# Optimization experiments

Hardware: AMD Instinct MI355X
Metric: run time of the kernel (lower is better)

The kernel has to match this reference:

```python
import jax, jax.numpy as jnp
import numpy as np

DIM = 1024
INTER = 512
E = 32            # n_routed_experts
TOPK = 4          # n_activated_experts
GROUPS = 8        # n_expert_groups
TOPK_GROUPS = 4
SHARED_INTER = 2 * INTER  # n_shared_experts * moe_inter_dim
ROUTE_SCALE = 1.0
B, S = 8, 4096


def setup_inputs() -> dict:
    key = jax.random.key(0)
    ks = jax.random.split(key, 16)
    def xav(k, shape):
        fan_in, fan_out = shape[-2], shape[-1]
        lim = np.sqrt(6.0 / (fan_in + fan_out))
        return jax.random.uniform(k, shape, jnp.float32, -lim, lim)
    return {
        "x": jax.random.normal(ks[0], (B, S, DIM), jnp.float32),
        "gw": xav(ks[1], (DIM, E)),
        "gb": jnp.zeros((E,), jnp.float32),
        "w1": xav(ks[2], (E, DIM, INTER)),
        "b1": jnp.zeros((E, INTER), jnp.float32),
        "w3": xav(ks[3], (E, DIM, INTER)),
        "b3": jnp.zeros((E, INTER), jnp.float32),
        "w2": xav(ks[4], (E, INTER, DIM)),
        "b2": jnp.zeros((E, DIM), jnp.float32),
        "sw1": xav(ks[5], (DIM, SHARED_INTER)),
        "sb1": jnp.zeros((SHARED_INTER,), jnp.float32),
        "sw3": xav(ks[6], (DIM, SHARED_INTER)),
        "sb3": jnp.zeros((SHARED_INTER,), jnp.float32),
        "sw2": xav(ks[7], (SHARED_INTER, DIM)),
        "sb2": jnp.zeros((DIM,), jnp.float32),
    }


def _gate(xf, gw, gb):
    # scores: softmax over routed experts in fp32 (score_func='softmax')
    T = xf.shape[0]
    scores = jax.nn.softmax((xf @ gw + gb).astype(jnp.float32), axis=-1)  # [T, E]
    original_scores = scores
    # group-masked routing (n_expert_groups > 1)
    scores_g = scores.reshape(T, GROUPS, E // GROUPS)                     # [T, G, E/G]
    group_scores = jnp.sum(jax.lax.top_k(scores_g, 2)[0], axis=-1)        # [T, G]
    gidx = jax.lax.top_k(group_scores, TOPK_GROUPS)[1]                    # [T, topk_groups]
    keep = jnp.zeros((T, GROUPS), bool).at[jnp.arange(T)[:, None], gidx].set(True)
    masked = jnp.where(keep[:, :, None], scores_g, -jnp.inf).reshape(T, E)
    indices = jax.lax.top_k(masked, TOPK)[1]                              # [T, topk]
    weights = jnp.take_along_axis(original_scores, indices, axis=1) * ROUTE_SCALE
    return weights.astype(xf.dtype), indices


def reference(x, gw, gb, w1, b1, w3, b3, w2, b2, sw1, sb1, sw3, sb3, sw2, sb2):
    shape = x.shape
    xf = x.reshape(-1, DIM)                                               # [T, dim]
    T = xf.shape[0]
    weights, indices = _gate(xf, gw, gb)
    # dense combine weights [T, E]: w_e(t) = routing weight if expert e chosen for t else 0
    cw = jnp.zeros((T, E), xf.dtype).at[jnp.arange(T)[:, None], indices].add(weights)
    # scan over experts: y += w_e * SwiGLU_e(x). Zero weight -> zero contribution,
    # identical math to the masked dispatch/scatter-add in the torch code.
    def body(y, p):
        w1e, b1e, w3e, b3e, w2e, b2e, we = p
        h = jax.nn.silu(xf @ w1e + b1e) * (xf @ w3e + b3e)                # [T, inter]
        return y + we[:, None] * (h @ w2e + b2e), None
    y0 = jnp.zeros_like(xf)
    y, _ = jax.lax.scan(body, y0, (w1, b1, w3, b3, w2, b2, cw.T))
    # shared experts MLP (SwiGLU)
    z = (jax.nn.silu(xf @ sw1 + sb1) * (xf @ sw3 + sb3)) @ sw2 + sb2
    return (y + z).reshape(shape)
```

## Files before the change

kernel.cpp:

```cpp
#include <hip/hip_runtime.h>
#include <stdint.h>

#define DIM_    1024
#define INTER_  512

typedef short bf16x4 __attribute__((ext_vector_type(4)));
typedef short bf16x8 __attribute__((ext_vector_type(8)));
typedef float f32x4  __attribute__((ext_vector_type(4)));

__device__ __forceinline__ unsigned short f2bf(float f) {
  union { float f; unsigned u; } v; v.f = f;
  return (unsigned short)((v.u + 0x7FFFu + ((v.u >> 16) & 1u)) >> 16);
}
__device__ __forceinline__ unsigned f2bf2(float a, float b) {
  union { float f; unsigned u; } va, vb; va.f = a; vb.f = b;
  unsigned ra = (va.u + 0x7FFFu + ((va.u >> 16) & 1u)) >> 16;
  unsigned rb = (vb.u + 0x7FFFu + ((vb.u >> 16) & 1u)) >> 16;
  return ra | (rb << 16);
}
__device__ __forceinline__ float bfhi(unsigned u) {
  union { unsigned u; float f; } v; v.u = u & 0xffff0000u; return v.f;
}
__device__ __forceinline__ float bflo(unsigned u) {
  union { unsigned u; float f; } v; v.u = u << 16; return v.f;
}
__device__ __forceinline__ int xorB(int j) { return (j & 7) ^ ((j >> 3) & 7); }

__device__ __forceinline__ void gl16(const void* g, void* l) {
  __builtin_amdgcn_global_load_lds(
      (const __attribute__((address_space(1))) unsigned int*)g,
      (__attribute__((address_space(3))) unsigned int*)l, 16, 0, 0);
}

__global__ __launch_bounds__(256) void gate_kernel(
    const float* __restrict__ x, const float* __restrict__ gw,
    const float* __restrict__ gb, int* __restrict__ idx, float* __restrict__ wts) {
  __shared__ double s_sc[4][32];
  __shared__ double s_gs[4][8];
  const int wid = threadIdx.x >> 6, lane = threadIdx.x & 63;
  const int t = blockIdx.x * 4 + wid;
  const int e = lane & 31, half = lane >> 5;
  const float* xr  = x  + (size_t)t * DIM_ + half * 512;
  const float* gwp = gw + (size_t)half * 512 * 32 + e;
  double a0 = 0, a1 = 0, a2 = 0, a3 = 0;
  for (int k = 0; k < 512; k += 4) {
    float4 xv = *(const float4*)(xr + k);
    a0 += (double)xv.x * (double)gwp[(k + 0) * 32];
    a1 += (double)xv.y * (double)gwp[(k + 1) * 32];
    a2 += (double)xv.z * (double)gwp[(k + 2) * 32];
    a3 += (double)xv.w * (double)gwp[(k + 3) * 32];
  }
  double lg = (a0 + a1) + (a2 + a3);
  lg += __shfl_xor(lg, 32);
  lg += (double)gb[e];
  double m = lg;
  #pragma unroll
  for (int d = 1; d < 32; d <<= 1) m = fmax(m, __shfl_xor(m, d));
  double ex = exp(lg - m);
  double ssum = ex;
  #pragma unroll
  for (int d = 1; d < 32; d <<= 1) ssum += __shfl_xor(ssum, d);
  double sc = ex / ssum;
  double p  = __shfl_xor(sc, 1);
  double m1 = fmax(sc, p), n1 = fmin(sc, p);
  double m2 = __shfl_xor(m1, 2), n2 = __shfl_xor(n1, 2);
  double gs = (m1 >= m2) ? (m1 + fmax(n1, m2)) : (m2 + fmax(n2, m1));
  if (lane < 32) {
    s_sc[wid][e] = sc;
    if ((e & 3) == 0) s_gs[wid][e >> 2] = gs;
  }
  __syncthreads();
  if (lane == 0) {
    unsigned kmask = 0;
    for (int it = 0; it < 4; ++it) {
      int bg = 0; double bv = -1.0;
      for (int g = 0; g < 8; ++g)
        if (!((kmask >> g) & 1u) && s_gs[wid][g] > bv) { bv = s_gs[wid][g]; bg = g; }
      kmask |= 1u << bg;
    }
    unsigned umask = 0;
    for (int slot = 0; slot < 4; ++slot) {
      int be = 0; double bv = -1.0;
      for (int ee = 0; ee < 32; ++ee)
        if (((kmask >> (ee >> 2)) & 1u) && !((umask >> ee) & 1u) && s_sc[wid][ee] > bv) {
          bv = s_sc[wid][ee]; be = ee;
        }
      umask |= 1u << be;
      idx[t * 4 + slot] = be;
      wts[t * 4 + slot] = (float)bv;
    }
  }
}

__global__ __launch_bounds__(256) void count_kernel(const int* __restrict__ idx,
                                                    int* __restrict__ meta) {
  __shared__ int h[32];
  int tid = threadIdx.x;
  if (tid < 32) h[tid] = 0;
  __syncthreads();
  atomicAdd(&h[idx[blockIdx.x * 256 + tid]], 1);
  __syncthreads();
  if (tid < 32 && h[tid]) atomicAdd(&meta[tid], h[tid]);
}

__global__ void scan_kernel(int* __restrict__ meta) {
  int lane = threadIdx.x & 63;
  if (lane < 32) {
    int c = meta[lane];
    int pre = c;
    #pragma unroll
    for (int d = 1; d < 32; d <<= 1) { int t = __shfl_up(pre, d); if (lane >= d) pre += t; }
    int excl = pre - c;
    meta[64 + lane] = excl;
    meta[32 + lane] = excl;
    int nt = (c + 127) >> 7;
    int ntp = nt;
    #pragma unroll
    for (int d = 1; d < 32; d <<= 1) { int t = __shfl_up(ntp, d); if (lane >= d) ntp += t; }
    int ntExcl = ntp - nt;
    for (int k = 0; k < nt; ++k) { meta[128 + ntExcl + k] = lane; meta[1184 + ntExcl + k] = k << 7; }
    if (lane == 31) { meta[96] = excl + c; meta[97] = ntExcl + nt; }
  }
}

__global__ __launch_bounds__(256) void scatter_kernel(
    const int* __restrict__ idx, int* __restrict__ meta,
    int* __restrict__ tok, int* __restrict__ inv) {
  int i = blockIdx.x * 256 + threadIdx.x;
  int lane = threadIdx.x & 63;
  int e = idx[i];
  unsigned long long m = ~0ull;
  #pragma unroll
  for (int b = 0; b < 5; ++b) {
    unsigned long long vote = __ballot((e >> b) & 1);
    m &= ((e >> b) & 1) ? vote : ~vote;
  }
  int leader = __ffsll((long long)m) - 1;
  int rank = __popcll(m & ((1ull << lane) - 1));
  int base = 0;
  if (lane == leader) base = atomicAdd(&meta[32 + e], (int)__popcll(m));
  base = __shfl(base, leader);
  int p = base + rank;
  tok[p] = i >> 2;
  inv[i] = p;
}

__global__ __launch_bounds__(256) void cvt_x_kernel(const float* __restrict__ x,
                                                    unsigned short* __restrict__ xb) {
  size_t i = ((size_t)blockIdx.x * 256 + threadIdx.x) * 8;
  float4 f0 = *(const float4*)(x + i);
  float4 f1 = *(const float4*)(x + i + 4);
  uint4 o;
  o.x = f2bf2(f0.x, f0.y); o.y = f2bf2(f0.z, f0.w);
  o.z = f2bf2(f1.x, f1.y); o.w = f2bf2(f1.z, f1.w);
  *(uint4*)(xb + i) = o;
}

__global__ __launch_bounds__(256) void repack_kernel(
    const float* __restrict__ src, unsigned short* __restrict__ dst,
    int K, int N, int tilesPerMat) {
  const int w = blockIdx.x * 4 + (threadIdx.x >> 6);
  const int l = threadIdx.x & 63;
  const int e = w / tilesPerMat, rem = w % tilesPerMat;
  const int kSteps = K >> 5;
  const int nt = rem / kSteps, kq = rem % kSteps;
  const float* s = src + (size_t)e * K * N + (size_t)(kq * 32) * N + nt * 64 + l;
  float v[32];
  #pragma unroll
  for (int kk = 0; kk < 32; ++kk) v[kk] = s[(size_t)kk * N];
  char* d = (char*)dst + (size_t)w * 4096 + l * 64;
  const int xb_ = xorB(l);
  #pragma unroll
  for (int q = 0; q < 8; ++q) {
    uint2 o;
    o.x = f2bf2(v[4 * q + 0], v[4 * q + 1]);
    o.y = f2bf2(v[4 * q + 2], v[4 * q + 3]);
    *(uint2*)(d + ((q ^ xb_) << 3)) = o;
  }
}

__global__ __launch_bounds__(256) void s1_kernel(
    const unsigned short* __restrict__ xb, const unsigned short* __restrict__ b1i,
    const unsigned short* __restrict__ b3i, const float* __restrict__ sb1,
    const float* __restrict__ sb3, unsigned short* __restrict__ Hs) {
  __shared__ char lds[32768];
  const int n0 = blockIdx.x * 64;
  const int m0 = blockIdx.y * 128;
  const int tid = threadIdx.x, lane = tid & 63, wave = tid >> 6;
  const int wm = wave >> 1, wn = wave & 1;

  const int r0 = tid >> 2, s0 = tid & 3;
  const int vrw = (r0 & 3) ^ ((r0 >> 2) & 1);
  const char* a0 = (const char*)xb + (size_t)(m0 + r0) * 2048 + ((s0 ^ vrw) << 4);
  const char* a1 = (const char*)xb + (size_t)(m0 + r0 + 64) * 2048 + ((s0 ^ vrw) << 4);
  const char* b1p = (const char*)b1i + (size_t)(blockIdx.x * 32) * 4096 + tid * 16;
  const char* b3p = (const char*)b3i + (size_t)(blockIdx.x * 32) * 4096 + tid * 16;

  const int g = lane >> 4;
  const int vfr = (lane & 3) ^ ((lane >> 2) & 1);
  const int aro = (wm * 64 + (lane & 15)) * 64 + ((g ^ vfr) << 4);
  int bofs[2];
  #pragma unroll
  for (int ni = 0; ni < 2; ++ni) {
    int j = wn * 32 + ni * 16 + (lane & 15);
    bofs[ni] = j * 64 + (((2 * g) ^ xorB(j)) << 3);
  }

  f32x4 acc1[4][2], acc3[4][2];
  const f32x4 zz = {0.f, 0.f, 0.f, 0.f};
  #pragma unroll
  for (int mi = 0; mi < 4; ++mi)
    #pragma unroll
    for (int ni = 0; ni < 2; ++ni) { acc1[mi][ni] = zz; acc3[mi][ni] = zz; }

  auto stage = [&](int buf, int kq) {
    char* b = lds + buf * 16384;
    gl16(a0 + kq * 64, b + wave * 1024);
    gl16(a1 + kq * 64, b + 4096 + wave * 1024);
    gl16(b1p + (size_t)kq * 4096, b + 8192 + wave * 1024);
    gl16(b3p + (size_t)kq * 4096, b + 12288 + wave * 1024);
  };
  stage(0, 0);
  __syncthreads();
  int cur = 0;
  for (int kq = 0; kq < 32; ++kq) {
    if (kq + 1 < 32) stage(cur ^ 1, kq + 1);
    char* cb = lds + cur * 16384;
    bf16x8 af[4];
    #pragma unroll
    for (int mi = 0; mi < 4; ++mi) af[mi] = *(const bf16x8*)(cb + aro + mi * 1024);
    #pragma unroll
    for (int ni = 0; ni < 2; ++ni) {
      bf16x4 lo = *(const bf16x4*)(cb + 8192 + bofs[ni]);
      bf16x4 hi = *(const bf16x4*)(cb + 8192 + (bofs[ni] ^ 8));
      bf16x8 bv = __builtin_shufflevector(lo, hi, 0, 1, 2, 3, 4, 5, 6, 7);
      #pragma unroll
      for (int mi = 0; mi < 4; ++mi)
        acc1[mi][ni] = __builtin_amdgcn_mfma_f32_16x16x32_bf16(af[mi], bv, acc1[mi][ni], 0, 0, 0);
      bf16x4 lo3 = *(const bf16x4*)(cb + 12288 + bofs[ni]);
      bf16x4 hi3 = *(const bf16x4*)(cb + 12288 + (bofs[ni] ^ 8));
      bf16x8 bv3 = __builtin_shufflevector(lo3, hi3, 0, 1, 2, 3, 4, 5, 6, 7);
      #pragma unroll
      for (int mi = 0; mi < 4; ++mi)
        acc3[mi][ni] = __builtin_amdgcn_mfma_f32_16x16x32_bf16(af[mi], bv3, acc3[mi][ni], 0, 0, 0);
    }
    __syncthreads();
    cur ^= 1;
  }
  #pragma unroll
  for (int ni = 0; ni < 2; ++ni) {
    int col = n0 + wn * 32 + ni * 16 + (lane & 15);
    float bb1 = sb1[col], bb3 = sb3[col];
    #pragma unroll
    for (int mi = 0; mi < 4; ++mi) {
      int rb = wm * 64 + mi * 16 + ((lane >> 4) << 2);
      #pragma unroll
      for (int r = 0; r < 4; ++r) {
        int row = m0 + rb + r;
        float v1 = acc1[mi][ni][r] + bb1;
        float v3 = acc3[mi][ni][r] + bb3;
        float h = (v1 / (1.f + __expf(-v1))) * v3;
        Hs[(size_t)row * 1024 + col] = f2bf(h);
      }
    }
  }
}

__global__ __launch_bounds__(256) void s2_kernel(
    const unsigned short* __restrict__ Hs, const unsigned short* __restrict__ b2i,
    const float* __restrict__ sb2, float* __restrict__ out) {
  __shared__ char lds[32768];
  const int n0 = blockIdx.x * 128;
  const int m0 = blockIdx.y * 128;
  const int tid = threadIdx.x, lane = tid & 63, wave = tid >> 6;
  const int wm = wave >> 1, wn = wave & 1;

  const int r0 = tid >> 2, s0 = tid & 3;
  const int vrw = (r0 & 3) ^ ((r0 >> 2) & 1);
  const char* a0 = (const char*)Hs + (size_t)(m0 + r0) * 2048 + ((s0 ^ vrw) << 4);
  const char* a1 = (const char*)Hs + (size_t)(m0 + r0 + 64) * 2048 + ((s0 ^ vrw) << 4);
  const char* bp0 = (const char*)b2i + (size_t)((blockIdx.x * 2 + 0) * 32) * 4096 + tid * 16;
  const char* bp1 = (const char*)b2i + (size_t)((blockIdx.x * 2 + 1) * 32) * 4096 + tid * 16;

  const int g = lane >> 4;
  const int vfr = (lane & 3) ^ ((lane >> 2) & 1);
  const int aro = (wm * 64 + (lane & 15)) * 64 + ((g ^ vfr) << 4);
  int bofs[4];
  #pragma unroll
  for (int ni = 0; ni < 4; ++ni) {
    int j = wn * 64 + ni * 16 + (lane & 15);
    bofs[ni] = j * 64 + (((2 * g) ^ xorB(j)) << 3);
  }
  f32x4 acc[4][4];
  const f32x4 zz = {0.f, 0.f, 0.f, 0.f};
  #pragma unroll
  for (int mi = 0; mi < 4; ++mi)
    #pragma unroll
    for (int ni = 0; ni < 4; ++ni) acc[mi][ni] = zz;

  auto stage = [&](int buf, int kq) {
    char* b = lds + buf * 16384;
    gl16(a0 + kq * 64, b + wave * 1024);
    gl16(a1 + kq * 64, b + 4096 + wave * 1024);
    gl16(bp0 + (size_t)kq * 4096, b + 8192 + wave * 1024);
    gl16(bp1 + (size_t)kq * 4096, b + 12288 + wave * 1024);
  };
  stage(0, 0);
  __syncthreads();
  int cur = 0;
  for (int kq = 0; kq < 32; ++kq) {
    if (kq + 1 < 32) stage(cur ^ 1, kq + 1);
    char* cb = lds + cur * 16384;
    bf16x8 af[4];
    #pragma unroll
    for (int mi = 0; mi < 4; ++mi) af[mi] = *(const bf16x8*)(cb + aro + mi * 1024);
    #pragma unroll
    for (int ni = 0; ni < 4; ++ni) {
      bf16x4 lo = *(const bf16x4*)(cb + 8192 + bofs[ni]);
      bf16x4 hi = *(const bf16x4*)(cb + 8192 + (bofs[ni] ^ 8));
      bf16x8 bv = __builtin_shufflevector(lo, hi, 0, 1, 2, 3, 4, 5, 6, 7);
      #pragma unroll
      for (int mi = 0; mi < 4; ++mi)
        acc[mi][ni] = __builtin_amdgcn_mfma_f32_16x16x32_bf16(af[mi], bv, acc[mi][ni], 0, 0, 0);
    }
    __syncthreads();
    cur ^= 1;
  }
  #pragma unroll
  for (int ni = 0; ni < 4; ++ni) {
    int col = n0 + wn * 64 + ni * 16 + (lane & 15);
    float bb = sb2[col];
    #pragma unroll
    for (int mi = 0; mi < 4; ++mi) {
      int rb = m0 + wm * 64 + mi * 16 + ((lane >> 4) << 2);
      #pragma unroll
      for (int r = 0; r < 4; ++r)
        out[(size_t)(rb + r) * 1024 + col] = acc[mi][ni][r] + bb;
    }
  }
}

__global__ __launch_bounds__(256) void g1_kernel(
    const unsigned short* __restrict__ xb, const unsigned short* __restrict__ w1i,
    const unsigned short* __restrict__ w3i, const float* __restrict__ b1,
    const float* __restrict__ b3, const int* __restrict__ tok,
    const int* __restrict__ meta, unsigned short* __restrict__ H) {
  __shared__ char lds[32768];
  if ((int)blockIdx.y >= meta[97]) return;
  const int e = meta[128 + blockIdx.y], m0 = meta[1184 + blockIdx.y];
  const int off_e = meta[64 + e], nrem = meta[e] - m0;
  const int n0 = blockIdx.x * 64;
  const int tid = threadIdx.x, lane = tid & 63, wave = tid >> 6;
  const int wm = wave >> 1, wn = wave & 1;

  const int r0 = tid >> 2, s0 = tid & 3;
  const int vrw = (r0 & 3) ^ ((r0 >> 2) & 1);
  int tr0 = tok[off_e + m0 + ((r0 < nrem) ? r0 : 0)];
  int tr1 = tok[off_e + m0 + ((r0 + 64 < nrem) ? r0 + 64 : 0)];
  const char* a0 = (const char*)xb + (size_t)tr0 * 2048 + ((s0 ^ vrw) << 4);
  const char* a1 = (const char*)xb + (size_t)tr1 * 2048 + ((s0 ^ vrw) << 4);
  const char* b1p = (const char*)w1i + (size_t)((e * 8 + blockIdx.x) * 32) * 4096 + tid * 16;
  const char* b3p = (const char*)w3i + (size_t)((e * 8 + blockIdx.x) * 32) * 4096 + tid * 16;

  const int g = lane >> 4;
  const int vfr = (lane & 3) ^ ((lane >> 2) & 1);
  const int aro = (wm * 64 + (lane & 15)) * 64 + ((g ^ vfr) << 4);
  int bofs[2];
  #pragma unroll
  for (int ni = 0; ni < 2; ++ni) {
    int j = wn * 32 + ni * 16 + (lane & 15);
    bofs[ni] = j * 64 + (((2 * g) ^ xorB(j)) << 3);
  }

  f32x4 acc1[4][2], acc3[4][2];
  const f32x4 zz = {0.f, 0.f, 0.f, 0.f};
  #pragma unroll
  for (int mi = 0; mi < 4; ++mi)
    #pragma unroll
    for (int ni = 0; ni < 2; ++ni) { acc1[mi][ni] = zz; acc3[mi][ni] = zz; }

  auto stage = [&](int buf, int kq) {
    char* b = lds + buf * 16384;
    gl16(a0 + kq * 64, b + wave * 1024);
    gl16(a1 + kq * 64, b + 4096 + wave * 1024);
    gl16(b1p + (size_t)kq * 4096, b + 8192 + wave * 1024);
    gl16(b3p + (size_t)kq * 4096, b + 12288 + wave * 1024);
  };
  stage(0, 0);
  __syncthreads();
  int cur = 0;
  for (int kq = 0; kq < 32; ++kq) {
    if (kq + 1 < 32) stage(cur ^ 1, kq + 1);
    char* cb = lds + cur * 16384;
    bf16x8 af[4];
    #pragma unroll
    for (int mi = 0; mi < 4; ++mi) af[mi] = *(const bf16x8*)(cb + aro + mi * 1024);
    #pragma unroll
    for (int ni = 0; ni < 2; ++ni) {
      bf16x4 lo = *(const bf16x4*)(cb + 8192 + bofs[ni]);
      bf16x4 hi = *(const bf16x4*)(cb + 8192 + (bofs[ni] ^ 8));
      bf16x8 bv = __builtin_shufflevector(lo, hi, 0, 1, 2, 3, 4, 5, 6, 7);
      #pragma unroll
      for (int mi = 0; mi < 4; ++mi)
        acc1[mi][ni] = __builtin_amdgcn_mfma_f32_16x16x32_bf16(af[mi], bv, acc1[mi][ni], 0, 0, 0);
      bf16x4 lo3 = *(const bf16x4*)(cb + 12288 + bofs[ni]);
      bf16x4 hi3 = *(const bf16x4*)(cb + 12288 + (bofs[ni] ^ 8));
      bf16x8 bv3 = __builtin_shufflevector(lo3, hi3, 0, 1, 2, 3, 4, 5, 6, 7);
      #pragma unroll
      for (int mi = 0; mi < 4; ++mi)
        acc3[mi][ni] = __builtin_amdgcn_mfma_f32_16x16x32_bf16(af[mi], bv3, acc3[mi][ni], 0, 0, 0);
    }
    __syncthreads();
    cur ^= 1;
  }
  #pragma unroll
  for (int ni = 0; ni < 2; ++ni) {
    int col = n0 + wn * 32 + ni * 16 + (lane & 15);
    float bb1 = b1[e * 512 + col], bb3 = b3[e * 512 + col];
    #pragma unroll
    for (int mi = 0; mi < 4; ++mi) {
      int rb = wm * 64 + mi * 16 + ((lane >> 4) << 2);
      #pragma unroll
      for (int r = 0; r < 4; ++r) {
        int row = rb + r;
        if (row < nrem) {
          float v1 = acc1[mi][ni][r] + bb1;
          float v3 = acc3[mi][ni][r] + bb3;
          float h = (v1 / (1.f + __expf(-v1))) * v3;
          H[(size_t)(off_e + m0 + row) * 512 + col] = f2bf(h);
        }
      }
    }
  }
}

__global__ __launch_bounds__(256) void g2_kernel(
    const unsigned short* __restrict__ H, const unsigned short* __restrict__ w2i,
    const float* __restrict__ b2, const int* __restrict__ meta,
    unsigned short* __restrict__ Y, int cbase) {
  __shared__ char lds[32768];
  if ((int)blockIdx.y >= meta[97]) return;
  const int e = meta[128 + blockIdx.y], m0 = meta[1184 + blockIdx.y];
  const int off_e = meta[64 + e], nrem = meta[e] - m0;
  const int n0 = cbase + blockIdx.x * 128;
  const int tid = threadIdx.x, lane = tid & 63, wave = tid >> 6;
  const int wm = wave >> 1, wn = wave & 1;

  const int r0 = tid >> 2, s0 = tid & 3;
  const int vrw = (r0 & 3) ^ ((r0 >> 2) & 1);
  const char* a0 = (const char*)H + (size_t)(off_e + m0 + ((r0 < nrem) ? r0 : 0)) * 1024 + ((s0 ^ vrw) << 4);
  const char* a1 = (const char*)H + (size_t)(off_e + m0 + ((r0 + 64 < nrem) ? r0 + 64 : 0)) * 1024 + ((s0 ^ vrw) << 4);
  const int ntb = n0 >> 6;
  const char* bp0 = (const char*)w2i + (size_t)((e * 16 + ntb + 0) * 16) * 4096 + tid * 16;
  const char* bp1 = (const char*)w2i + (size_t)((e * 16 + ntb + 1) * 16) * 4096 + tid * 16;

  const int g = lane >> 4;
  const int vfr = (lane & 3) ^ ((lane >> 2) & 1);
  const int aro = (wm * 64 + (lane & 15)) * 64 + ((g ^ vfr) << 4);
  int bofs[4];
  #pragma unroll
  for (int ni = 0; ni < 4; ++ni) {
    int j = wn * 64 + ni * 16 + (lane & 15);
    bofs[ni] = j * 64 + (((2 * g) ^ xorB(j)) << 3);
  }
  f32x4 acc[4][4];
  const f32x4 zz = {0.f, 0.f, 0.f, 0.f};
  #pragma unroll
  for (int mi = 0; mi < 4; ++mi)
    #pragma unroll
    for (int ni = 0; ni < 4; ++ni) acc[mi][ni] = zz;

  auto stage = [&](int buf, int kq) {
    char* b = lds + buf * 16384;
    gl16(a0 + kq * 64, b + wave * 1024);
    gl16(a1 + kq * 64, b + 4096 + wave * 1024);
    gl16(bp0 + (size_t)kq * 4096, b + 8192 + wave * 1024);
    gl16(bp1 + (size_t)kq * 4096, b + 12288 + wave * 1024);
  };
  stage(0, 0);
  __syncthreads();
  int cur = 0;
  for (int kq = 0; kq < 16; ++kq) {
    if (kq + 1 < 16) stage(cur ^ 1, kq + 1);
    char* cb = lds + cur * 16384;
    bf16x8 af[4];
    #pragma unroll
    for (int mi = 0; mi < 4; ++mi) af[mi] = *(const bf16x8*)(cb + aro + mi * 1024);
    #pragma unroll
    for (int ni = 0; ni < 4; ++ni) {
      bf16x4 lo = *(const bf16x4*)(cb + 8192 + bofs[ni]);
      bf16x4 hi = *(const bf16x4*)(cb + 8192 + (bofs[ni] ^ 8));
      bf16x8 bv = __builtin_shufflevector(lo, hi, 0, 1, 2, 3, 4, 5, 6, 7);
      #pragma unroll
      for (int mi = 0; mi < 4; ++mi)
        acc[mi][ni] = __builtin_amdgcn_mfma_f32_16x16x32_bf16(af[mi], bv, acc[mi][ni], 0, 0, 0);
    }
    __syncthreads();
    cur ^= 1;
  }
  #pragma unroll
  for (int ni = 0; ni < 4; ++ni) {
    int col = n0 + wn * 64 + ni * 16 + (lane & 15);
    float bb = b2[e * 1024 + col];
    int ycol = col - cbase;
    #pragma unroll
    for (int mi = 0; mi < 4; ++mi) {
      int rb = wm * 64 + mi * 16 + ((lane >> 4) << 2);
      #pragma unroll
      for (int r = 0; r < 4; ++r) {
        int row = rb + r;
        if (row < nrem)
          Y[(size_t)(off_e + m0 + row) * 512 + ycol] = f2bf(acc[mi][ni][r] + bb);
      }
    }
  }
}

__global__ __launch_bounds__(256) void combine_kernel(
    const unsigned short* __restrict__ Y, const int* __restrict__ inv,
    const float* __restrict__ wts, float* __restrict__ out, int cbase) {
  int t = blockIdx.x * 2 + (threadIdx.x >> 7);
  int c = (threadIdx.x & 127) * 4;
  int4 iv = *(const int4*)(inv + t * 4);
  float4 wv = *(const float4*)(wts + t * 4);
  float* op = out + (size_t)t * 1024 + cbase + c;
  float4 o = *(float4*)op;
  uint2 u;
  u = *(const uint2*)(Y + (size_t)iv.x * 512 + c);
  o.x += wv.x * bflo(u.x); o.y += wv.x * bfhi(u.x);
  o.z += wv.x * bflo(u.y); o.w += wv.x * bfhi(u.y);
  u = *(const uint2*)(Y + (size_t)iv.y * 512 + c);
  o.x += wv.y * bflo(u.x); o.y += wv.y * bfhi(u.x);
  o.z += wv.y * bflo(u.y); o.w += wv.y * bfhi(u.y);
  u = *(const uint2*)(Y + (size_t)iv.z * 512 + c);
  o.x += wv.z * bflo(u.x); o.y += wv.z * bfhi(u.x);
  o.z += wv.z * bflo(u.y); o.w += wv.z * bfhi(u.y);
  u = *(const uint2*)(Y + (size_t)iv.w * 512 + c);
  o.x += wv.w * bflo(u.x); o.y += wv.w * bfhi(u.x);
  o.z += wv.w * bflo(u.y); o.w += wv.w * bfhi(u.y);
  *(float4*)op = o;
}

extern "C" void kernel_launch(void* const* d_in, const int* in_sizes, int n_in,
                              void* d_out, int out_size, void* d_ws, size_t ws_size,
                              hipStream_t stream) {
  const float* x   = (const float*)d_in[0];
  const float* gw  = (const float*)d_in[1];
  const float* gb  = (const float*)d_in[2];
  const float* w1  = (const float*)d_in[3];
  const float* b1  = (const float*)d_in[4];
  const float* w3  = (const float*)d_in[5];
  const float* b3  = (const float*)d_in[6];
  const float* w2  = (const float*)d_in[7];
  const float* b2  = (const float*)d_in[8];
  const float* sw1 = (const float*)d_in[9];
  const float* sb1 = (const float*)d_in[10];
  const float* sw3 = (const float*)d_in[11];
  const float* sb3 = (const float*)d_in[12];
  const float* sw2 = (const float*)d_in[13];
  const float* sb2 = (const float*)d_in[14];
  float* out = (float*)d_out;
  char* ws = (char*)d_ws;

  const size_t OFF_XB   = 134217728;
  const size_t OFF_W1I  = 201326592;
  const size_t OFF_W3I  = 234881024;
  const size_t OFF_W2I  = 268435456;
  const size_t OFF_SW1I = 301989888;
  const size_t OFF_SW3I = 304087040;
  const size_t OFF_SW2I = 306184192;
  const size_t OFF_IDX  = 308281344;
  const size_t OFF_WTS  = 308805632;
  const size_t OFF_TOK  = 309329920;
  const size_t OFF_INV  = 309854208;
  const size_t OFF_META = 310378496;
  if (ws_size < OFF_META + 8960) return;

  unsigned short* H    = (unsigned short*)ws;
  unsigned short* xb   = (unsigned short*)(ws + OFF_XB);
  unsigned short* Yb   = (unsigned short*)(ws + OFF_XB);
  unsigned short* w1i  = (unsigned short*)(ws + OFF_W1I);
  unsigned short* w3i  = (unsigned short*)(ws + OFF_W3I);
  unsigned short* w2i  = (unsigned short*)(ws + OFF_W2I);
  unsigned short* sw1i = (unsigned short*)(ws + OFF_SW1I);
  unsigned short* sw3i = (unsigned short*)(ws + OFF_SW3I);
  unsigned short* sw2i = (unsigned short*)(ws + OFF_SW2I);
  int*   idx  = (int*)(ws + OFF_IDX);
  float* wts  = (float*)(ws + OFF_WTS);
  int*   tokl = (int*)(ws + OFF_TOK);
  int*   inv  = (int*)(ws + OFF_INV);
  int*   meta = (int*)(ws + OFF_META);

  hipMemsetAsync(meta, 0, 128, stream);
  gate_kernel<<<dim3(8192), dim3(256), 0, stream>>>(x, gw, gb, idx, wts);
  count_kernel<<<dim3(512), dim3(256), 0, stream>>>(idx, meta);
  scan_kernel<<<dim3(1), dim3(64), 0, stream>>>(meta);
  scatter_kernel<<<dim3(512), dim3(256), 0, stream>>>(idx, meta, tokl, inv);
  cvt_x_kernel<<<dim3(16384), dim3(256), 0, stream>>>(x, xb);
  repack_kernel<<<dim3(2048), dim3(256), 0, stream>>>(w1, w1i, 1024, 512, 256);
  repack_kernel<<<dim3(2048), dim3(256), 0, stream>>>(w3, w3i, 1024, 512, 256);
  repack_kernel<<<dim3(2048), dim3(256), 0, stream>>>(w2, w2i, 512, 1024, 256);
  repack_kernel<<<dim3(128), dim3(256), 0, stream>>>(sw1, sw1i, 1024, 1024, 512);
  repack_kernel<<<dim3(128), dim3(256), 0, stream>>>(sw3, sw3i, 1024, 1024, 512);
  repack_kernel<<<dim3(128), dim3(256), 0, stream>>>(sw2, sw2i, 1024, 1024, 512);
  s1_kernel<<<dim3(16, 256), dim3(256), 0, stream>>>(xb, sw1i, sw3i, sb1, sb3, H);
  s2_kernel<<<dim3(8, 256), dim3(256), 0, stream>>>(H, sw2i, sb2, out);
  g1_kernel<<<dim3(8, 1056), dim3(256), 0, stream>>>(xb, w1i, w3i, b1, b3, tokl, meta, H);
  g2_kernel<<<dim3(4, 1056), dim3(256), 0, stream>>>(H, w2i, b2, meta, Yb, 0);
  combine_kernel<<<dim3(16384), dim3(256), 0, stream>>>(Yb, inv, wts, out, 0);
  g2_kernel<<<dim3(4, 1056), dim3(256), 0, stream>>>(H, w2i, b2, meta, Yb, 512);
  combine_kernel<<<dim3(16384), dim3(256), 0, stream>>>(Yb, inv, wts, out, 512);
}
```

Baseline: 1.605 ms.

## Fuse x bf16 conversion into gate kernel and switch B tiles to 16-byte swizzle

The fp32-to-bf16 conversion of x now happens inside the gate kernel, which already reads each token row, so the separate cvt_x launch and its second full read of x are gone. The weight repack now writes 16-byte chunks with a 2-bit XOR swizzle. The GEMM kernels' B-fragment reads change from two 8-byte LDS loads plus a shuffle to one 16-byte load. The s2/g2 offsets are also recomputed for the two 64-column B halves. This lowers LDS instruction count and global traffic, but the new swizzle may bring back some LDS bank conflicts.

```diff
diff --git a/kernel.cpp b/kernel.cpp
--- a/kernel.cpp
+++ b/kernel.cpp
@@ -24,7 +24,6 @@
 __device__ __forceinline__ float bflo(unsigned u) {
   union { unsigned u; float f; } v; v.u = u << 16; return v.f;
 }
-__device__ __forceinline__ int xorB(int j) { return (j & 7) ^ ((j >> 3) & 7); }
 
 __device__ __forceinline__ void gl16(const void* g, void* l) {
   __builtin_amdgcn_global_load_lds(
@@ -34,11 +33,27 @@
 
 __global__ __launch_bounds__(256) void gate_kernel(
     const float* __restrict__ x, const float* __restrict__ gw,
-    const float* __restrict__ gb, int* __restrict__ idx, float* __restrict__ wts) {
+    const float* __restrict__ gb, int* __restrict__ idx, float* __restrict__ wts,
+    unsigned short* __restrict__ xb) {
   __shared__ double s_sc[4][32];
   __shared__ double s_gs[4][8];
   const int wid = threadIdx.x >> 6, lane = threadIdx.x & 63;
   const int t = blockIdx.x * 4 + wid;
+  {
+    const float* xrow = x + (size_t)t * DIM_ + lane * 16;
+    unsigned short* xbrow = xb + (size_t)t * DIM_ + lane * 16;
+    float4 f0 = *(const float4*)(xrow);
+    float4 f1 = *(const float4*)(xrow + 4);
+    float4 f2v = *(const float4*)(xrow + 8);
+    float4 f3v = *(const float4*)(xrow + 12);
+    uint4 o0, o1;
+    o0.x = f2bf2(f0.x, f0.y);  o0.y = f2bf2(f0.z, f0.w);
+    o0.z = f2bf2(f1.x, f1.y);  o0.w = f2bf2(f1.z, f1.w);
+    o1.x = f2bf2(f2v.x, f2v.y); o1.y = f2bf2(f2v.z, f2v.w);
+    o1.z = f2bf2(f3v.x, f3v.y); o1.w = f2bf2(f3v.z, f3v.w);
+    *(uint4*)(xbrow) = o0;
+    *(uint4*)(xbrow + 8) = o1;
+  }
   const int e = lane & 31, half = lane >> 5;
   const float* xr  = x  + (size_t)t * DIM_ + half * 512;
   const float* gwp = gw + (size_t)half * 512 * 32 + e;
@@ -145,37 +160,29 @@
   inv[i] = p;
 }
 
-__global__ __launch_bounds__(256) void cvt_x_kernel(const float* __restrict__ x,
-                                                    unsigned short* __restrict__ xb) {
-  size_t i = ((size_t)blockIdx.x * 256 + threadIdx.x) * 8;
-  float4 f0 = *(const float4*)(x + i);
-  float4 f1 = *(const float4*)(x + i + 4);
-  uint4 o;
-  o.x = f2bf2(f0.x, f0.y); o.y = f2bf2(f0.z, f0.w);
-  o.z = f2bf2(f1.x, f1.y); o.w = f2bf2(f1.z, f1.w);
-  *(uint4*)(xb + i) = o;
-}
-
 __global__ __launch_bounds__(256) void repack_kernel(
     const float* __restrict__ src, unsigned short* __restrict__ dst,
     int K, int N, int tilesPerMat) {
   const int w = blockIdx.x * 4 + (threadIdx.x >> 6);
-  const int l = threadIdx.x & 63;
+  const int j = threadIdx.x & 63;
   const int e = w / tilesPerMat, rem = w % tilesPerMat;
   const int kSteps = K >> 5;
   const int nt = rem / kSteps, kq = rem % kSteps;
-  const float* s = src + (size_t)e * K * N + (size_t)(kq * 32) * N + nt * 64 + l;
+  const float* s = src + (size_t)e * K * N + (size_t)(kq * 32) * N + nt * 64 + j;
   float v[32];
   #pragma unroll
   for (int kk = 0; kk < 32; ++kk) v[kk] = s[(size_t)kk * N];
-  char* d = (char*)dst + (size_t)w * 4096 + l * 64;
-  const int xb_ = xorB(l);
-  #pragma unroll
-  for (int q = 0; q < 8; ++q) {
-    uint2 o;
-    o.x = f2bf2(v[4 * q + 0], v[4 * q + 1]);
-    o.y = f2bf2(v[4 * q + 2], v[4 * q + 3]);
-    *(uint2*)(d + ((q ^ xb_) << 3)) = o;
+  char* d = (char*)dst + (size_t)w * 4096 + j * 64;
+  const int sz = (j & 3) ^ ((j >> 2) & 3);
+  #pragma unroll
+  for (int q = 0; q < 4; ++q) {
+    int o = (q ^ sz) * 8;
+    uint4 tv;
+    tv.x = f2bf2(v[o + 0], v[o + 1]);
+    tv.y = f2bf2(v[o + 2], v[o + 3]);
+    tv.z = f2bf2(v[o + 4], v[o + 5]);
+    tv.w = f2bf2(v[o + 6], v[o + 7]);
+    *(uint4*)(d + q * 16) = tv;
   }
 }
 
@@ -203,7 +210,8 @@
   #pragma unroll
   for (int ni = 0; ni < 2; ++ni) {
     int j = wn * 32 + ni * 16 + (lane & 15);
-    bofs[ni] = j * 64 + (((2 * g) ^ xorB(j)) << 3);
+    int sz = (j & 3) ^ ((j >> 2) & 3);
+    bofs[ni] = j * 64 + ((g ^ sz) << 4);
   }
 
   f32x4 acc1[4][2], acc3[4][2];
@@ -231,15 +239,11 @@
     for (int mi = 0; mi < 4; ++mi) af[mi] = *(const bf16x8*)(cb + aro + mi * 1024);
     #pragma unroll
     for (int ni = 0; ni < 2; ++ni) {
-      bf16x4 lo = *(const bf16x4*)(cb + 8192 + bofs[ni]);
-      bf16x4 hi = *(const bf16x4*)(cb + 8192 + (bofs[ni] ^ 8));
-      bf16x8 bv = __builtin_shufflevector(lo, hi, 0, 1, 2, 3, 4, 5, 6, 7);
+      bf16x8 bv = *(const bf16x8*)(cb + 8192 + bofs[ni]);
       #pragma unroll
       for (int mi = 0; mi < 4; ++mi)
         acc1[mi][ni] = __builtin_amdgcn_mfma_f32_16x16x32_bf16(af[mi], bv, acc1[mi][ni], 0, 0, 0);
-      bf16x4 lo3 = *(const bf16x4*)(cb + 12288 + bofs[ni]);
-      bf16x4 hi3 = *(const bf16x4*)(cb + 12288 + (bofs[ni] ^ 8));
-      bf16x8 bv3 = __builtin_shufflevector(lo3, hi3, 0, 1, 2, 3, 4, 5, 6, 7);
+      bf16x8 bv3 = *(const bf16x8*)(cb + 12288 + bofs[ni]);
       #pragma unroll
       for (int mi = 0; mi < 4; ++mi)
         acc3[mi][ni] = __builtin_amdgcn_mfma_f32_16x16x32_bf16(af[mi], bv3, acc3[mi][ni], 0, 0, 0);
@@ -289,7 +293,8 @@
   #pragma unroll
   for (int ni = 0; ni < 4; ++ni) {
     int j = wn * 64 + ni * 16 + (lane & 15);
-    bofs[ni] = j * 64 + (((2 * g) ^ xorB(j)) << 3);
+    int sz = (j & 3) ^ ((j >> 2) & 3);
+    bofs[ni] = 8192 + (j >> 6) * 4096 + (j & 63) * 64 + ((g ^ sz) << 4);
   }
   f32x4 acc[4][4];
   const f32x4 zz = {0.f, 0.f, 0.f, 0.f};
@@ -316,9 +321,7 @@
     for (int mi = 0; mi < 4; ++mi) af[mi] = *(const bf16x8*)(cb + aro + mi * 1024);
     #pragma unroll
     for (int ni = 0; ni < 4; ++ni) {
-      bf16x4 lo = *(const bf16x4*)(cb + 8192 + bofs[ni]);
-      bf16x4 hi = *(const bf16x4*)(cb + 8192 + (bofs[ni] ^ 8));
-      bf16x8 bv = __builtin_shufflevector(lo, hi, 0, 1, 2, 3, 4, 5, 6, 7);
+      bf16x8 bv = *(const bf16x8*)(cb + bofs[ni]);
       #pragma unroll
       for (int mi = 0; mi < 4; ++mi)
         acc[mi][ni] = __builtin_amdgcn_mfma_f32_16x16x32_bf16(af[mi], bv, acc[mi][ni], 0, 0, 0);
@@ -369,7 +372,8 @@
   #pragma unroll
   for (int ni = 0; ni < 2; ++ni) {
     int j = wn * 32 + ni * 16 + (lane & 15);
-    bofs[ni] = j * 64 + (((2 * g) ^ xorB(j)) << 3);
+    int sz = (j & 3) ^ ((j >> 2) & 3);
+    bofs[ni] = j * 64 + ((g ^ sz) << 4);
   }
 
   f32x4 acc1[4][2], acc3[4][2];
@@ -397,15 +401,11 @@
     for (int mi = 0; mi < 4; ++mi) af[mi] = *(const bf16x8*)(cb + aro + mi * 1024);
     #pragma unroll
     for (int ni = 0; ni < 2; ++ni) {
-      bf16x4 lo = *(const bf16x4*)(cb + 8192 + bofs[ni]);
-      bf16x4 hi = *(const bf16x4*)(cb + 8192 + (bofs[ni] ^ 8));
-      bf16x8 bv = __builtin_shufflevector(lo, hi, 0, 1, 2, 3, 4, 5, 6, 7);
+      bf16x8 bv = *(const bf16x8*)(cb + 8192 + bofs[ni]);
       #pragma unroll
       for (int mi = 0; mi < 4; ++mi)
         acc1[mi][ni] = __builtin_amdgcn_mfma_f32_16x16x32_bf16(af[mi], bv, acc1[mi][ni], 0, 0, 0);
-      bf16x4 lo3 = *(const bf16x4*)(cb + 12288 + bofs[ni]);
-      bf16x4 hi3 = *(const bf16x4*)(cb + 12288 + (bofs[ni] ^ 8));
-      bf16x8 bv3 = __builtin_shufflevector(lo3, hi3, 0, 1, 2, 3, 4, 5, 6, 7);
+      bf16x8 bv3 = *(const bf16x8*)(cb + 12288 + bofs[ni]);
       #pragma unroll
       for (int mi = 0; mi < 4; ++mi)
         acc3[mi][ni] = __builtin_amdgcn_mfma_f32_16x16x32_bf16(af[mi], bv3, acc3[mi][ni], 0, 0, 0);
@@ -461,7 +461,8 @@
   #pragma unroll
   for (int ni = 0; ni < 4; ++ni) {
     int j = wn * 64 + ni * 16 + (lane & 15);
-    bofs[ni] = j * 64 + (((2 * g) ^ xorB(j)) << 3);
+    int sz = (j & 3) ^ ((j >> 2) & 3);
+    bofs[ni] = 8192 + (j >> 6) * 4096 + (j & 63) * 64 + ((g ^ sz) << 4);
   }
   f32x4 acc[4][4];
   const f32x4 zz = {0.f, 0.f, 0.f, 0.f};
@@ -488,9 +489,7 @@
     for (int mi = 0; mi < 4; ++mi) af[mi] = *(const bf16x8*)(cb + aro + mi * 1024);
     #pragma unroll
     for (int ni = 0; ni < 4; ++ni) {
-      bf16x4 lo = *(const bf16x4*)(cb + 8192 + bofs[ni]);
-      bf16x4 hi = *(const bf16x4*)(cb + 8192 + (bofs[ni] ^ 8));
-      bf16x8 bv = __builtin_shufflevector(lo, hi, 0, 1, 2, 3, 4, 5, 6, 7);
+      bf16x8 bv = *(const bf16x8*)(cb + bofs[ni]);
       #pragma unroll
       for (int mi = 0; mi < 4; ++mi)
         acc[mi][ni] = __builtin_amdgcn_mfma_f32_16x16x32_bf16(af[mi], bv, acc[mi][ni], 0, 0, 0);
@@ -592,11 +591,10 @@
   int*   meta = (int*)(ws + OFF_META);
 
   hipMemsetAsync(meta, 0, 128, stream);
-  gate_kernel<<<dim3(8192), dim3(256), 0, stream>>>(x, gw, gb, idx, wts);
+  gate_kernel<<<dim3(8192), dim3(256), 0, stream>>>(x, gw, gb, idx, wts, xb);
   count_kernel<<<dim3(512), dim3(256), 0, stream>>>(idx, meta);
   scan_kernel<<<dim3(1), dim3(64), 0, stream>>>(meta);
   scatter_kernel<<<dim3(512), dim3(256), 0, stream>>>(idx, meta, tokl, inv);
-  cvt_x_kernel<<<dim3(16384), dim3(256), 0, stream>>>(x, xb);
   repack_kernel<<<dim3(2048), dim3(256), 0, stream>>>(w1, w1i, 1024, 512, 256);
   repack_kernel<<<dim3(2048), dim3(256), 0, stream>>>(w3, w3i, 1024, 512, 256);
   repack_kernel<<<dim3(2048), dim3(256), 0, stream>>>(w2, w2i, 512, 1024, 256);
```

After: 1.605 ms. About the same (+0.0%).
